# Kernel tuning notes

Measured on AMD Instinct MI355X. Metric: run time of the kernel, lower is better.

Reference implementation:

```python
import jax, jax.numpy as jnp
import numpy as np

B, D, T = 32, 256, 2048
L, K = 8, 1024


def setup_inputs() -> dict:
    key = jax.random.key(0)
    k1, k2 = jax.random.split(key)
    x = jax.random.normal(k1, (B, D, T), dtype=jnp.float32)
    codebooks = jax.random.normal(k2, (L, K, D), dtype=jnp.float32)
    return {"x": x, "codebooks": codebooks}


def reference(x, codebooks):
    """Residual VQ: per layer, cdist + argmin + gather, subtract, accumulate.

    x: (B, D, T) latents; codebooks: (L, K, D).
    Returns (output (B, D, T), indices (B, L, T)).
    """
    b, d, t = x.shape
    r0 = jnp.transpose(x, (0, 2, 1)).reshape(-1, d)  # (N, D), N = B*T

    def step(residual, W):
        # squared euclidean distance: |r|^2 - 2 r.W^T + |W|^2  -> (N, K)
        dist2 = (jnp.sum(residual * residual, axis=-1, keepdims=True)
                 - 2.0 * residual @ W.T
                 + jnp.sum(W * W, axis=-1))
        idx = jnp.argmin(dist2, axis=-1)          # (N,)
        q = W[idx]                                 # gather (N, D)
        return residual - q, (q, idx)

    _, (qs, idxs) = jax.lax.scan(step, r0, codebooks)
    out = jnp.sum(qs, axis=0).reshape(b, t, d)     # sum over layers
    out = jnp.transpose(out, (0, 2, 1))            # (B, D, T)
    indices = jnp.transpose(idxs.reshape(codebooks.shape[0], b, t), (1, 0, 2))  # (B, L, T)
    return out, indices
```

## Files before the change

### kernel.cpp

```cpp
#include <hip/hip_runtime.h>
#include <cmath>

constexpr int Bb = 32, Dd = 256, Tt = 2048, Ll = 8, Kk = 1024;
constexpr int VT = 64;
constexpr int KT = 64;
constexpr int ROWU = 264;
constexpr int TILE_USH = KT * ROWU;
constexpr int TILE_BYTES = TILE_USH * 2;
constexpr int CHUNKS = TILE_BYTES / 1024;
constexpr int CSTR = 48;

typedef __attribute__((ext_vector_type(8))) short short8;
typedef __attribute__((ext_vector_type(4))) float f32x4;

__device__ __forceinline__ ushort f2bf(float x) {
    union { float f; uint32_t u; } v{x};
    uint32_t r = v.u + 0x7fffu + ((v.u >> 16) & 1u);
    return (ushort)(r >> 16);
}
__device__ __forceinline__ float bf2f(ushort h) {
    union { uint32_t u; float f; } v{((uint32_t)h) << 16};
    return v.f;
}
__device__ __forceinline__ void gl_lds16(const void* g, void* l) {
    __builtin_amdgcn_global_load_lds(
        (const __attribute__((address_space(1))) unsigned int*)g,
        (__attribute__((address_space(3))) unsigned int*)l, 16, 0, 0);
}

__global__ void prep_kernel(const float* __restrict__ cb, float* __restrict__ wn,
                            ushort* __restrict__ sp) {
    const int code = blockIdx.x;
    const int lane = threadIdx.x;
    const int l = code >> 10, kk = code & 1023, kt = kk >> 6, kr = kk & 63;
    const float4 v = ((const float4*)(cb + (size_t)code * Dd))[lane];
    float s = v.x * v.x + v.y * v.y + v.z * v.z + v.w * v.w;
#pragma unroll
    for (int off = 32; off > 0; off >>= 1) s += __shfl_down(s, off, 64);
    if (lane == 0) wn[code] = s;

    float f[4] = {v.x, v.y, v.z, v.w};
    ushort hs[4];
#pragma unroll
    for (int i = 0; i < 4; ++i) hs[i] = f2bf(f[i]);
    ushort* base = sp + (size_t)(l * 16 + kt) * TILE_USH + kr * ROWU + lane * 4;
    *(ushort4*)base = make_ushort4(hs[0], hs[1], hs[2], hs[3]);
}

__launch_bounds__(256, 2)
__global__ void rvq_kernel(const float* __restrict__ x, const float* __restrict__ cb,
                           const float* __restrict__ wn, const ushort* __restrict__ sp,
                           float* __restrict__ out, float* __restrict__ oidx) {
    __shared__ __align__(16) ushort Btile[2 * TILE_USH];
    __shared__ int   sidx[VT];
    __shared__ int   cnt[VT];
    __shared__ int   cand[VT * CSTR];

    const int tid = threadIdx.x;
    const int w = tid >> 6, lane = tid & 63;
    const int c = lane & 15;
    const int q = lane >> 4;
    const int b = blockIdx.x >> 5, t0 = (blockIdx.x & 31) * VT;
    const int myrow = 16 * w + c;
    const int t_a = t0 + myrow;

    float R_[8][8];
    {
        const float* xb = x + (size_t)b * Dd * Tt + t_a;
#pragma unroll
        for (int s = 0; s < 8; ++s)
#pragma unroll
            for (int j = 0; j < 8; ++j)
                R_[s][j] = xb[(size_t)(32 * s + 8 * q + j) * Tt];
    }

    for (int l = 0; l < Ll; ++l) {
        const float*  cbl = cb + (size_t)l * Kk * Dd;
        const float*  wnl = wn + l * Kk;
        const ushort* spl = sp + (size_t)l * 16 * TILE_USH;

        short8 ah[8], al[8];
#pragma unroll
        for (int s = 0; s < 8; ++s)
#pragma unroll
            for (int j = 0; j < 8; ++j) {
                float v = R_[s][j];
                ushort h = f2bf(v);
                ah[s][j] = (short)h;
                al[s][j] = (short)f2bf(v - bf2f(h));
            }

        float d1[4], d2[4], d3[4]; int i1[4], i2[4], i3[4];
#pragma unroll
        for (int i = 0; i < 4; ++i) {
            d1[i] = __builtin_inff(); d2[i] = __builtin_inff(); d3[i] = __builtin_inff();
            i1[i] = 0; i2[i] = 0; i3[i] = 0;
        }

        auto STAGE = [&](int kt, int buf) {
            const char* gsrc = (const char*)spl + (size_t)kt * TILE_BYTES;
            char* ldst = (char*)(Btile + buf * TILE_USH);
            for (int ch = w; ch < CHUNKS; ch += 4)
                gl_lds16(gsrc + ch * 1024 + lane * 16, ldst + ch * 1024);
        };

        STAGE(0, 0);
        for (int kt = 0; kt < 16; ++kt) {
            __syncthreads();
            if (kt < 15) STAGE(kt + 1, (kt + 1) & 1);

            const ushort* bt = Btile + (kt & 1) * TILE_USH;

            float wnv[4];
#pragma unroll
            for (int sub = 0; sub < 4; ++sub) wnv[sub] = wnl[kt * 64 + sub * 16 + c];

            f32x4 hh[4], lh[4];
#pragma unroll
            for (int sub = 0; sub < 4; ++sub) { hh[sub] = (f32x4)0.f; lh[sub] = (f32x4)0.f; }

#pragma unroll
            for (int s = 0; s < 8; ++s) {
                const ushort* bp = bt + s * 32 + q * 8;
                short8 bf[4];
#pragma unroll
                for (int sub = 0; sub < 4; ++sub)
                    bf[sub] = *(const short8*)(bp + (sub * 16 + c) * ROWU);
#pragma unroll
                for (int sub = 0; sub < 4; ++sub)
                    hh[sub] = __builtin_amdgcn_mfma_f32_16x16x32_bf16(ah[s], bf[sub], hh[sub], 0, 0, 0);
#pragma unroll
                for (int sub = 0; sub < 4; ++sub)
                    lh[sub] = __builtin_amdgcn_mfma_f32_16x16x32_bf16(al[s], bf[sub], lh[sub], 0, 0, 0);
            }
#pragma unroll
            for (int sub = 0; sub < 4; ++sub) {
                const int kbase = kt * 64 + sub * 16 + c;
#pragma unroll
                for (int i = 0; i < 4; ++i) {
                    float acc = hh[sub][i] + lh[sub][i];
                    float d = fmaf(-2.f, acc, wnv[sub]);
                    bool lt1 = d < d1[i], lt2 = d < d2[i], lt3 = d < d3[i];
                    d3[i] = lt2 ? d2[i] : (lt3 ? d : d3[i]);
                    i3[i] = lt2 ? i2[i] : (lt3 ? kbase : i3[i]);
                    d2[i] = lt1 ? d1[i] : (lt2 ? d : d2[i]);
                    i2[i] = lt1 ? i1[i] : (lt2 ? kbase : i2[i]);
                    d1[i] = lt1 ? d : d1[i];
                    i1[i] = lt1 ? kbase : i1[i];
                }
            }
        }

        __syncthreads();
        float* Rcp = (float*)Btile;
        {
            float* dst = Rcp + myrow * ROWU + 8 * q;
#pragma unroll
            for (int s = 0; s < 8; ++s) {
                float4 lo4 = {R_[s][0], R_[s][1], R_[s][2], R_[s][3]};
                float4 hi4 = {R_[s][4], R_[s][5], R_[s][6], R_[s][7]};
                *(float4*)(dst + 32 * s)     = lo4;
                *(float4*)(dst + 32 * s + 4) = hi4;
            }
        }
        if (tid < VT) cnt[tid] = 0;

        float bmin[4];
#pragma unroll
        for (int i = 0; i < 4; ++i) {
            float md = d1[i];
#pragma unroll
            for (int off = 1; off < 16; off <<= 1) {
                float od = __shfl_xor(md, off, 64);
                md = od < md ? od : md;
            }
            bmin[i] = md;
        }
        __syncthreads();

#pragma unroll
        for (int i = 0; i < 4; ++i) {
            const int row = 16 * w + 4 * q + i;
            const float thr = bmin[i] + 1.0f;
            if (d1[i] <= thr) { int s_ = atomicAdd(&cnt[row], 1); cand[row * CSTR + s_] = i1[i]; }
            if (d2[i] <= thr) { int s_ = atomicAdd(&cnt[row], 1); cand[row * CSTR + s_] = i2[i]; }
            if (d3[i] <= thr) { int s_ = atomicAdd(&cnt[row], 1); cand[row * CSTR + s_] = i3[i]; }
        }
        __syncthreads();

        if (tid < VT) {
            const int row = tid;
            const int n = cnt[row];
            int bi = cand[row * CSTR];
            if (n > 1) {
                const float* rp = Rcp + row * ROWU;
                float rn = 0.f;
                for (int i = 0; i < Dd / 4; ++i) {
                    float4 r4 = *(const float4*)(rp + 4 * i);
                    rn += r4.x * r4.x + r4.y * r4.y + r4.z * r4.z + r4.w * r4.w;
                }
                float bd = __builtin_inff(); bi = 0x7fffffff;
                for (int j = 0; j < n; ++j) {
                    const int cc = cand[row * CSTR + j];
                    const float* wp = cbl + (size_t)cc * Dd;
                    float dot = 0.f;
                    for (int d = 0; d < Dd; ++d)
                        dot = fmaf(rp[d], wp[d], dot);
                    const float dist = (rn - 2.0f * dot) + wnl[cc];
                    if (dist < bd || (dist == bd && cc < bi)) { bd = dist; bi = cc; }
                }
            }
            sidx[row] = bi;
            oidx[((size_t)b * Ll + l) * Tt + t0 + row] = (float)bi;
        }
        __syncthreads();

        {
            const int cc = sidx[myrow];
            const float* wp = cbl + (size_t)cc * Dd + 8 * q;
#pragma unroll
            for (int s = 0; s < 8; ++s) {
                float4 w0 = *(const float4*)(wp + 32 * s);
                float4 w1 = *(const float4*)(wp + 32 * s + 4);
                R_[s][0] -= w0.x; R_[s][1] -= w0.y; R_[s][2] -= w0.z; R_[s][3] -= w0.w;
                R_[s][4] -= w1.x; R_[s][5] -= w1.y; R_[s][6] -= w1.z; R_[s][7] -= w1.w;
            }
        }
    }

    {
        const float* xb = x + (size_t)b * Dd * Tt + t_a;
        float* ob = out + (size_t)b * Dd * Tt + t_a;
#pragma unroll
        for (int s = 0; s < 8; ++s)
#pragma unroll
            for (int j = 0; j < 8; ++j) {
                size_t off = (size_t)(32 * s + 8 * q + j) * Tt;
                ob[off] = xb[off] - R_[s][j];
            }
    }
}

extern "C" void kernel_launch(void* const* d_in, const int* in_sizes, int n_in,
                              void* d_out, int out_size, void* d_ws, size_t ws_size,
                              hipStream_t stream) {
    const float* x  = (const float*)d_in[0];
    const float* cb = (const float*)d_in[1];
    float* out  = (float*)d_out;
    float* oidx = out + (size_t)Bb * Dd * Tt;
    float*  wnbuf = (float*)d_ws;
    ushort* spbuf = (ushort*)((char*)d_ws + 32768);

    prep_kernel<<<Ll * Kk, 64, 0, stream>>>(cb, wnbuf, spbuf);
    rvq_kernel<<<(Bb * Tt) / VT, 256, 0, stream>>>(x, cb, wnbuf, spbuf, out, oidx);
}
```

Measured before the change: 976.7 us.

## Split codebook subtiles across two wave groups with 512-thread blocks

Doubles the block to 512 threads so two groups of four waves each handle half of the 64-code subtile columns for the same 64 rows. Each group keeps its own top-3 candidates, and the per-row minimum is combined through shared memory. The candidate buffer is halved, and a bounds check falls back to a full codebook scan if it overflows. This aims to raise wave occupancy and hide MFMA/LDS latency, at the cost of duplicated residual registers, duplicated bf16 splitting, and more barriers per tile.

```diff
diff --git a/kernel.cpp b/kernel.cpp
--- a/kernel.cpp
+++ b/kernel.cpp
@@ -8,7 +8,7 @@
 constexpr int TILE_USH = KT * ROWU;
 constexpr int TILE_BYTES = TILE_USH * 2;
 constexpr int CHUNKS = TILE_BYTES / 1024;
-constexpr int CSTR = 48;
+constexpr int CSTR = 24;
 
 typedef __attribute__((ext_vector_type(8))) short short8;
 typedef __attribute__((ext_vector_type(4))) float f32x4;
@@ -47,21 +47,24 @@
     *(ushort4*)base = make_ushort4(hs[0], hs[1], hs[2], hs[3]);
 }
 
-__launch_bounds__(256, 2)
+__launch_bounds__(512, 4)
 __global__ void rvq_kernel(const float* __restrict__ x, const float* __restrict__ cb,
                            const float* __restrict__ wn, const ushort* __restrict__ sp,
                            float* __restrict__ out, float* __restrict__ oidx) {
     __shared__ __align__(16) ushort Btile[2 * TILE_USH];
     __shared__ int   sidx[VT];
     __shared__ int   cnt[VT];
+    __shared__ float bminW[2][VT];
     __shared__ int   cand[VT * CSTR];
 
     const int tid = threadIdx.x;
     const int w = tid >> 6, lane = tid & 63;
+    const int wl = w & 3;
+    const int g  = w >> 2;
     const int c = lane & 15;
     const int q = lane >> 4;
     const int b = blockIdx.x >> 5, t0 = (blockIdx.x & 31) * VT;
-    const int myrow = 16 * w + c;
+    const int myrow = 16 * wl + c;
     const int t_a = t0 + myrow;
 
     float R_[8][8];
@@ -100,7 +103,7 @@
         auto STAGE = [&](int kt, int buf) {
             const char* gsrc = (const char*)spl + (size_t)kt * TILE_BYTES;
             char* ldst = (char*)(Btile + buf * TILE_USH);
-            for (int ch = w; ch < CHUNKS; ch += 4)
+            for (int ch = w; ch < CHUNKS; ch += 8)
                 gl_lds16(gsrc + ch * 1024 + lane * 16, ldst + ch * 1024);
         };
 
@@ -111,35 +114,32 @@
 
             const ushort* bt = Btile + (kt & 1) * TILE_USH;
 
-            float wnv[4];
-#pragma unroll
-            for (int sub = 0; sub < 4; ++sub) wnv[sub] = wnl[kt * 64 + sub * 16 + c];
-
-            f32x4 hh[4], lh[4];
-#pragma unroll
-            for (int sub = 0; sub < 4; ++sub) { hh[sub] = (f32x4)0.f; lh[sub] = (f32x4)0.f; }
+            float wnv[2];
+#pragma unroll
+            for (int subl = 0; subl < 2; ++subl)
+                wnv[subl] = wnl[kt * 64 + (2 * g + subl) * 16 + c];
+
+            f32x4 hh[2], lh[2];
+#pragma unroll
+            for (int subl = 0; subl < 2; ++subl) { hh[subl] = (f32x4)0.f; lh[subl] = (f32x4)0.f; }
 
 #pragma unroll
             for (int s = 0; s < 8; ++s) {
                 const ushort* bp = bt + s * 32 + q * 8;
-                short8 bf[4];
-#pragma unroll
-                for (int sub = 0; sub < 4; ++sub)
-                    bf[sub] = *(const short8*)(bp + (sub * 16 + c) * ROWU);
-#pragma unroll
-                for (int sub = 0; sub < 4; ++sub)
-                    hh[sub] = __builtin_amdgcn_mfma_f32_16x16x32_bf16(ah[s], bf[sub], hh[sub], 0, 0, 0);
-#pragma unroll
-                for (int sub = 0; sub < 4; ++sub)
-                    lh[sub] = __builtin_amdgcn_mfma_f32_16x16x32_bf16(al[s], bf[sub], lh[sub], 0, 0, 0);
-            }
-#pragma unroll
-            for (int sub = 0; sub < 4; ++sub) {
-                const int kbase = kt * 64 + sub * 16 + c;
+                short8 bf0 = *(const short8*)(bp + ((2 * g + 0) * 16 + c) * ROWU);
+                short8 bf1 = *(const short8*)(bp + ((2 * g + 1) * 16 + c) * ROWU);
+                hh[0] = __builtin_amdgcn_mfma_f32_16x16x32_bf16(ah[s], bf0, hh[0], 0, 0, 0);
+                hh[1] = __builtin_amdgcn_mfma_f32_16x16x32_bf16(ah[s], bf1, hh[1], 0, 0, 0);
+                lh[0] = __builtin_amdgcn_mfma_f32_16x16x32_bf16(al[s], bf0, lh[0], 0, 0, 0);
+                lh[1] = __builtin_amdgcn_mfma_f32_16x16x32_bf16(al[s], bf1, lh[1], 0, 0, 0);
+            }
+#pragma unroll
+            for (int subl = 0; subl < 2; ++subl) {
+                const int kbase = kt * 64 + (2 * g + subl) * 16 + c;
 #pragma unroll
                 for (int i = 0; i < 4; ++i) {
-                    float acc = hh[sub][i] + lh[sub][i];
-                    float d = fmaf(-2.f, acc, wnv[sub]);
+                    float acc = hh[subl][i] + lh[subl][i];
+                    float d = fmaf(-2.f, acc, wnv[subl]);
                     bool lt1 = d < d1[i], lt2 = d < d2[i], lt3 = d < d3[i];
                     d3[i] = lt2 ? d2[i] : (lt3 ? d : d3[i]);
                     i3[i] = lt2 ? i2[i] : (lt3 ? kbase : i3[i]);
@@ -153,7 +153,7 @@
 
         __syncthreads();
         float* Rcp = (float*)Btile;
-        {
+        if (g == 0) {
             float* dst = Rcp + myrow * ROWU + 8 * q;
 #pragma unroll
             for (int s = 0; s < 8; ++s) {
@@ -176,15 +176,19 @@
             }
             bmin[i] = md;
         }
+        if (c == 0) {
+#pragma unroll
+            for (int i = 0; i < 4; ++i) bminW[g][16 * wl + 4 * q + i] = bmin[i];
+        }
         __syncthreads();
 
 #pragma unroll
         for (int i = 0; i < 4; ++i) {
-            const int row = 16 * w + 4 * q + i;
-            const float thr = bmin[i] + 1.0f;
-            if (d1[i] <= thr) { int s_ = atomicAdd(&cnt[row], 1); cand[row * CSTR + s_] = i1[i]; }
-            if (d2[i] <= thr) { int s_ = atomicAdd(&cnt[row], 1); cand[row * CSTR + s_] = i2[i]; }
-            if (d3[i] <= thr) { int s_ = atomicAdd(&cnt[row], 1); cand[row * CSTR + s_] = i3[i]; }
+            const int row = 16 * wl + 4 * q + i;
+            const float thr = fminf(bminW[0][row], bminW[1][row]) + 1.0f;
+            if (d1[i] <= thr) { int s_ = atomicAdd(&cnt[row], 1); if (s_ < CSTR) cand[row * CSTR + s_] = i1[i]; }
+            if (d2[i] <= thr) { int s_ = atomicAdd(&cnt[row], 1); if (s_ < CSTR) cand[row * CSTR + s_] = i2[i]; }
+            if (d3[i] <= thr) { int s_ = atomicAdd(&cnt[row], 1); if (s_ < CSTR) cand[row * CSTR + s_] = i3[i]; }
         }
         __syncthreads();
 
@@ -199,9 +203,11 @@
                     float4 r4 = *(const float4*)(rp + 4 * i);
                     rn += r4.x * r4.x + r4.y * r4.y + r4.z * r4.z + r4.w * r4.w;
                 }
+                const bool ovf = n > CSTR;
+                const int m = ovf ? Kk : n;
                 float bd = __builtin_inff(); bi = 0x7fffffff;
-                for (int j = 0; j < n; ++j) {
-                    const int cc = cand[row * CSTR + j];
+                for (int j = 0; j < m; ++j) {
+                    const int cc = ovf ? j : cand[row * CSTR + j];
                     const float* wp = cbl + (size_t)cc * Dd;
                     float dot = 0.f;
                     for (int d = 0; d < Dd; ++d)
@@ -228,7 +234,7 @@
         }
     }
 
-    {
+    if (g == 0) {
         const float* xb = x + (size_t)b * Dd * Tt + t_a;
         float* ob = out + (size_t)b * Dd * Tt + t_a;
 #pragma unroll
@@ -252,5 +258,5 @@
     ushort* spbuf = (ushort*)((char*)d_ws + 32768);
 
     prep_kernel<<<Ll * Kk, 64, 0, stream>>>(cb, wnbuf, spbuf);
-    rvq_kernel<<<(Bb * Tt) / VT, 256, 0, stream>>>(x, cb, wnbuf, spbuf, out, oidx);
-}
+    rvq_kernel<<<(Bb * Tt) / VT, 512, 0, stream>>>(x, cb, wnbuf, spbuf, out, oidx);
+}
```

Result: slower. 1.661 ms (+70.1%).
